# Performance work log

Measured on AMD Instinct MI355X. Metric: run time of the kernel, lower is better.

The kernel has to match this reference:

```python
import jax, jax.numpy as jnp
import numpy as np

EPS = 1e-8
N = 4
B = 1_000_000


def setup_inputs() -> dict:
    key = jax.random.key(0)
    g = jax.random.normal(key, (B, N, N), dtype=jnp.float32)
    # SPD covariance-like matrices: G G^T + 0.1 I (well-conditioned, distinct eigvals)
    x = jnp.einsum('bik,bjk->bij', g, g) / N + 0.1 * jnp.eye(N, dtype=jnp.float32)
    return {"x": x}


def reference(x):
    # 1) symmetrize + epsilon regularization (ensure SPD)
    sym = 0.5 * (x + jnp.swapaxes(x, -1, -2)) + EPS * jnp.eye(N, dtype=x.dtype)
    # 2) exact matrix log via eigendecomposition
    w, v = jnp.linalg.eigh(sym)                      # w: [B, N], v: [B, N, N]
    log_w = jnp.log(jnp.maximum(w, EPS))
    logm = jnp.einsum('bik,bk,bjk->bij', v, log_w, v)  # V diag(log w) V^T
    # 3) re-symmetrize
    logm = 0.5 * (logm + jnp.swapaxes(logm, -1, -2))
    # 4) upper-triangular vectorization, row-major (i, j>=i) order
    iu, ju = jnp.triu_indices(N)
    return logm[:, iu, ju]                           # [B, N*(N+1)//2]
```

## Files before the change

### kernel.cpp

```cpp
#include <hip/hip_runtime.h>
#include <math.h>

#ifndef NSWEEP
#define NSWEEP 4
#endif

#define EPSV 1e-8f

__device__ __forceinline__ float fast_sqrtf(float x) {
#if __has_builtin(__builtin_amdgcn_sqrtf)
  return __builtin_amdgcn_sqrtf(x);
#else
  return sqrtf(x);
#endif
}
__device__ __forceinline__ float fast_rcpf(float x) {
#if __has_builtin(__builtin_amdgcn_rcpf)
  return __builtin_amdgcn_rcpf(x);
#else
  return 1.0f / x;
#endif
}
__device__ __forceinline__ float fast_rsqf(float x) {
#if __has_builtin(__builtin_amdgcn_rsqf)
  return __builtin_amdgcn_rsqf(x);
#else
  return rsqrtf(x);
#endif
}
__device__ __forceinline__ float fast_logf(float x) {
#if __has_builtin(__builtin_amdgcn_logf)
  return __builtin_amdgcn_logf(x) * 0.6931471805599453f;
#else
  return logf(x);
#endif
}

#define JROT(APP, AQQ, APQ, AK1P, AK1Q, AK2P, AK2Q,                       \
             VP0, VQ0, VP1, VQ1, VP2, VQ2, VP3, VQ3)                      \
  do {                                                                    \
    float a_ = APQ;                                                       \
    float d_ = AQQ - APP;                                                 \
    float a2_ = a_ + a_;                                                  \
    float r_ = fast_sqrtf(fmaf(d_, d_, a2_ * a2_));                       \
    float den_ = fmaxf(fabsf(d_) + r_, 1e-30f);                          \
    float num_ = __int_as_float(__float_as_int(a2_) ^                     \
                                (__float_as_int(d_) & 0x80000000));       \
    float t_ = num_ * fast_rcpf(den_);                                    \
    float c_ = fast_rsqf(fmaf(t_, t_, 1.0f));                             \
    float s_ = t_ * c_;                                                   \
    float ta_ = t_ * a_;                                                  \
    APP = APP - ta_;                                                      \
    AQQ = AQQ + ta_;                                                      \
    APQ = 0.0f;                                                           \
    { float kp_ = AK1P, kq_ = AK1Q;                                       \
      AK1P = fmaf(c_, kp_, -s_ * kq_);                                    \
      AK1Q = fmaf(s_, kp_, c_ * kq_); }                                   \
    { float kp_ = AK2P, kq_ = AK2Q;                                       \
      AK2P = fmaf(c_, kp_, -s_ * kq_);                                    \
      AK2Q = fmaf(s_, kp_, c_ * kq_); }                                   \
    { float p_ = VP0, q_ = VQ0;                                           \
      VP0 = fmaf(c_, p_, -s_ * q_);                                       \
      VQ0 = fmaf(s_, p_, c_ * q_); }                                      \
    { float p_ = VP1, q_ = VQ1;                                           \
      VP1 = fmaf(c_, p_, -s_ * q_);                                       \
      VQ1 = fmaf(s_, p_, c_ * q_); }                                      \
    { float p_ = VP2, q_ = VQ2;                                           \
      VP2 = fmaf(c_, p_, -s_ * q_);                                       \
      VQ2 = fmaf(s_, p_, c_ * q_); }                                      \
    { float p_ = VP3, q_ = VQ3;                                           \
      VP3 = fmaf(c_, p_, -s_ * q_);                                       \
      VQ3 = fmaf(s_, p_, c_ * q_); }                                      \
  } while (0)

__device__ __forceinline__ void logm_one(float4 r0, float4 r1, float4 r2,
                                         float4 r3, float o[10]) {
  float a00 = r0.x + EPSV;
  float a01 = 0.5f * (r0.y + r1.x);
  float a02 = 0.5f * (r0.z + r2.x);
  float a03 = 0.5f * (r0.w + r3.x);
  float a11 = r1.y + EPSV;
  float a12 = 0.5f * (r1.z + r2.y);
  float a13 = 0.5f * (r1.w + r3.y);
  float a22 = r2.z + EPSV;
  float a23 = 0.5f * (r2.w + r3.z);
  float a33 = r3.w + EPSV;

  float v00 = 1.f, v01 = 0.f, v02 = 0.f, v03 = 0.f;
  float v10 = 0.f, v11 = 1.f, v12 = 0.f, v13 = 0.f;
  float v20 = 0.f, v21 = 0.f, v22 = 1.f, v23 = 0.f;
  float v30 = 0.f, v31 = 0.f, v32 = 0.f, v33 = 1.f;

#pragma unroll 1
  for (int sweep = 0; sweep < NSWEEP; ++sweep) {
    JROT(a00, a11, a01, a02, a12, a03, a13,
         v00, v01, v10, v11, v20, v21, v30, v31);
    JROT(a00, a22, a02, a01, a12, a03, a23,
         v00, v02, v10, v12, v20, v22, v30, v32);
    JROT(a00, a33, a03, a01, a13, a02, a23,
         v00, v03, v10, v13, v20, v23, v30, v33);
    JROT(a11, a22, a12, a01, a02, a13, a23,
         v01, v02, v11, v12, v21, v22, v31, v32);
    JROT(a11, a33, a13, a01, a03, a12, a23,
         v01, v03, v11, v13, v21, v23, v31, v33);
    JROT(a22, a33, a23, a02, a03, a12, a13,
         v02, v03, v12, v13, v22, v23, v32, v33);
  }

  float lw0 = fast_logf(fmaxf(a00, EPSV));
  float lw1 = fast_logf(fmaxf(a11, EPSV));
  float lw2 = fast_logf(fmaxf(a22, EPSV));
  float lw3 = fast_logf(fmaxf(a33, EPSV));

  float w00 = v00 * lw0, w01 = v01 * lw1, w02 = v02 * lw2, w03 = v03 * lw3;
  float w10 = v10 * lw0, w11 = v11 * lw1, w12 = v12 * lw2, w13 = v13 * lw3;
  float w20 = v20 * lw0, w21 = v21 * lw1, w22 = v22 * lw2, w23 = v23 * lw3;
  float w30 = v30 * lw0, w31 = v31 * lw1, w32 = v32 * lw2, w33 = v33 * lw3;

  o[0] = fmaf(w00, v00, fmaf(w01, v01, fmaf(w02, v02, w03 * v03)));
  o[1] = fmaf(w00, v10, fmaf(w01, v11, fmaf(w02, v12, w03 * v13)));
  o[2] = fmaf(w00, v20, fmaf(w01, v21, fmaf(w02, v22, w03 * v23)));
  o[3] = fmaf(w00, v30, fmaf(w01, v31, fmaf(w02, v32, w03 * v33)));
  o[4] = fmaf(w10, v10, fmaf(w11, v11, fmaf(w12, v12, w13 * v13)));
  o[5] = fmaf(w10, v20, fmaf(w11, v21, fmaf(w12, v22, w13 * v23)));
  o[6] = fmaf(w10, v30, fmaf(w11, v31, fmaf(w12, v32, w13 * v33)));
  o[7] = fmaf(w20, v20, fmaf(w21, v21, fmaf(w22, v22, w23 * v23)));
  o[8] = fmaf(w20, v30, fmaf(w21, v31, fmaf(w22, v32, w23 * v33)));
  o[9] = fmaf(w30, v30, fmaf(w31, v31, fmaf(w32, v32, w33 * v33)));
}

__global__ __launch_bounds__(256) void TangentSpaceLayer_64141041598486_kernel(
    const float* __restrict__ x, float* __restrict__ out, int B) {
  __shared__ __align__(16) float so[512 * 10];
  const int t = threadIdx.x;
  const int base = blockIdx.x * 512;
  const int m0 = min(base + t, B - 1);
  const int m1 = min(base + 256 + t, B - 1);

  const float* p0 = x + (size_t)m0 * 16;
  const float* p1 = x + (size_t)m1 * 16;
  float4 a0 = *(const float4*)(p0 + 0);
  float4 a1 = *(const float4*)(p0 + 4);
  float4 a2 = *(const float4*)(p0 + 8);
  float4 a3 = *(const float4*)(p0 + 12);
  float4 b0 = *(const float4*)(p1 + 0);
  float4 b1 = *(const float4*)(p1 + 4);
  float4 b2 = *(const float4*)(p1 + 8);
  float4 b3 = *(const float4*)(p1 + 12);

  float oA[10], oB[10];
  logm_one(a0, a1, a2, a3, oA);
  logm_one(b0, b1, b2, b3, oB);

  float* spA = so + t * 10;
  float* spB = so + (t + 256) * 10;
#pragma unroll
  for (int i = 0; i < 10; ++i) spA[i] = oA[i];
#pragma unroll
  for (int i = 0; i < 10; ++i) spB[i] = oB[i];

  __syncthreads();

  const int valid = min(512, B - blockIdx.x * 512);
  const int nf = valid * 10;
  const int n4 = nf >> 2;
  float* obase = out + (size_t)blockIdx.x * 5120;
  const float4* s4 = (const float4*)so;
  float4* o4 = (float4*)obase;
  for (int i = t; i < n4; i += 256) o4[i] = s4[i];
  for (int i = n4 * 4 + t; i < nf; i += 256) obase[i] = so[i];
}

extern "C" void kernel_launch(void* const* d_in, const int* in_sizes, int n_in,
                              void* d_out, int out_size, void* d_ws, size_t ws_size,
                              hipStream_t stream) {
  const float* x = (const float*)d_in[0];
  float* out = (float*)d_out;
  const int B = in_sizes[0] / 16;
  const int blocks = (B + 511) / 512;
  hipLaunchKernelGGL(TangentSpaceLayer_64141041598486_kernel, dim3(blocks),
                     dim3(256), 0, stream, x, out, B);
}
```

Measured before the change: 113.4 us.

## Interleave three matrices per thread and use rsqrt-only Jacobi rotation

Each thread now processes three 4x4 matrices instead of two, and each Jacobi rotation step is interleaved across the three matrices to expose independent instruction-level parallelism. The rotation formula is also rewritten to derive c and s from two reciprocal square roots, replacing the sqrt and rcp calls. This aims to hide transcendental latency and cut the cost per rotation. In exchange it raises register pressure (about 78 live floats per thread), launches fewer blocks, and uses a larger shared-memory staging buffer.

```diff
diff --git a/kernel.cpp b/kernel.cpp
--- a/kernel.cpp
+++ b/kernel.cpp
@@ -6,21 +6,10 @@
 #endif
 
 #define EPSV 1e-8f
+#define NM 3
+#define BT 256
+#define MPB (NM * BT)
 
-__device__ __forceinline__ float fast_sqrtf(float x) {
-#if __has_builtin(__builtin_amdgcn_sqrtf)
-  return __builtin_amdgcn_sqrtf(x);
-#else
-  return sqrtf(x);
-#endif
-}
-__device__ __forceinline__ float fast_rcpf(float x) {
-#if __has_builtin(__builtin_amdgcn_rcpf)
-  return __builtin_amdgcn_rcpf(x);
-#else
-  return 1.0f / x;
-#endif
-}
 __device__ __forceinline__ float fast_rsqf(float x) {
 #if __has_builtin(__builtin_amdgcn_rsqf)
   return __builtin_amdgcn_rsqf(x);
@@ -36,139 +25,149 @@
 #endif
 }
 
-#define JROT(APP, AQQ, APQ, AK1P, AK1Q, AK2P, AK2Q,                       \
-             VP0, VQ0, VP1, VQ1, VP2, VQ2, VP3, VQ3)                      \
-  do {                                                                    \
-    float a_ = APQ;                                                       \
-    float d_ = AQQ - APP;                                                 \
-    float a2_ = a_ + a_;                                                  \
-    float r_ = fast_sqrtf(fmaf(d_, d_, a2_ * a2_));                       \
-    float den_ = fmaxf(fabsf(d_) + r_, 1e-30f);                          \
-    float num_ = __int_as_float(__float_as_int(a2_) ^                     \
-                                (__float_as_int(d_) & 0x80000000));       \
-    float t_ = num_ * fast_rcpf(den_);                                    \
-    float c_ = fast_rsqf(fmaf(t_, t_, 1.0f));                             \
-    float s_ = t_ * c_;                                                   \
-    float ta_ = t_ * a_;                                                  \
-    APP = APP - ta_;                                                      \
-    AQQ = AQQ + ta_;                                                      \
-    APQ = 0.0f;                                                           \
-    { float kp_ = AK1P, kq_ = AK1Q;                                       \
-      AK1P = fmaf(c_, kp_, -s_ * kq_);                                    \
-      AK1Q = fmaf(s_, kp_, c_ * kq_); }                                   \
-    { float kp_ = AK2P, kq_ = AK2Q;                                       \
-      AK2P = fmaf(c_, kp_, -s_ * kq_);                                    \
-      AK2Q = fmaf(s_, kp_, c_ * kq_); }                                   \
-    { float p_ = VP0, q_ = VQ0;                                           \
-      VP0 = fmaf(c_, p_, -s_ * q_);                                       \
-      VQ0 = fmaf(s_, p_, c_ * q_); }                                      \
-    { float p_ = VP1, q_ = VQ1;                                           \
-      VP1 = fmaf(c_, p_, -s_ * q_);                                       \
-      VQ1 = fmaf(s_, p_, c_ * q_); }                                      \
-    { float p_ = VP2, q_ = VQ2;                                           \
-      VP2 = fmaf(c_, p_, -s_ * q_);                                       \
-      VQ2 = fmaf(s_, p_, c_ * q_); }                                      \
-    { float p_ = VP3, q_ = VQ3;                                           \
-      VP3 = fmaf(c_, p_, -s_ * q_);                                       \
-      VQ3 = fmaf(s_, p_, c_ * q_); }                                      \
+#define JROT(APP, AQQ, APQ, AK1P, AK1Q, AK2P, AK2Q,                         \
+             VP0, VQ0, VP1, VQ1, VP2, VQ2, VP3, VQ3)                        \
+  do {                                                                      \
+    float aa_ = APQ;                                                        \
+    float d_ = AQQ - APP;                                                   \
+    float a2_ = aa_ + aa_;                                                  \
+    float r2_ = fmaf(d_, d_, a2_ * a2_);                                    \
+    float h_ = fast_rsqf(fmaxf(r2_, 1e-30f));                               \
+    float p_ = fabsf(d_) * h_;                                              \
+    p_ = (r2_ <= 1e-30f) ? 1.0f : p_;                                       \
+    float q_ = fmaf(2.0f, p_, 2.0f);                                        \
+    float ri_ = fast_rsqf(q_);                                              \
+    float c_ = q_ * (0.5f * ri_);                                           \
+    float n_ = __int_as_float(__float_as_int(a2_ * h_) ^                    \
+                              (__float_as_int(d_) & 0x80000000));           \
+    float s_ = n_ * ri_;                                                    \
+    float t_ = (n_ + n_) * (ri_ * ri_);                                     \
+    float ta_ = t_ * aa_;                                                   \
+    APP = APP - ta_;                                                        \
+    AQQ = AQQ + ta_;                                                        \
+    APQ = 0.0f;                                                             \
+    { float kp_ = AK1P, kq_ = AK1Q;                                         \
+      AK1P = fmaf(c_, kp_, -s_ * kq_);                                      \
+      AK1Q = fmaf(s_, kp_, c_ * kq_); }                                     \
+    { float kp_ = AK2P, kq_ = AK2Q;                                         \
+      AK2P = fmaf(c_, kp_, -s_ * kq_);                                      \
+      AK2Q = fmaf(s_, kp_, c_ * kq_); }                                     \
+    { float p0_ = VP0, q0_ = VQ0;                                           \
+      VP0 = fmaf(c_, p0_, -s_ * q0_);                                       \
+      VQ0 = fmaf(s_, p0_, c_ * q0_); }                                      \
+    { float p0_ = VP1, q0_ = VQ1;                                           \
+      VP1 = fmaf(c_, p0_, -s_ * q0_);                                       \
+      VQ1 = fmaf(s_, p0_, c_ * q0_); }                                      \
+    { float p0_ = VP2, q0_ = VQ2;                                           \
+      VP2 = fmaf(c_, p0_, -s_ * q0_);                                       \
+      VQ2 = fmaf(s_, p0_, c_ * q0_); }                                      \
+    { float p0_ = VP3, q0_ = VQ3;                                           \
+      VP3 = fmaf(c_, p0_, -s_ * q0_);                                       \
+      VQ3 = fmaf(s_, p0_, c_ * q0_); }                                      \
   } while (0)
 
-__device__ __forceinline__ void logm_one(float4 r0, float4 r1, float4 r2,
-                                         float4 r3, float o[10]) {
-  float a00 = r0.x + EPSV;
-  float a01 = 0.5f * (r0.y + r1.x);
-  float a02 = 0.5f * (r0.z + r2.x);
-  float a03 = 0.5f * (r0.w + r3.x);
-  float a11 = r1.y + EPSV;
-  float a12 = 0.5f * (r1.z + r2.y);
-  float a13 = 0.5f * (r1.w + r3.y);
-  float a22 = r2.z + EPSV;
-  float a23 = 0.5f * (r2.w + r3.z);
-  float a33 = r3.w + EPSV;
+#define ROT_01(m) JROT(A[m][0], A[m][4], A[m][1], A[m][2], A[m][5],         \
+                       A[m][3], A[m][6], V[m][0], V[m][1], V[m][4],         \
+                       V[m][5], V[m][8], V[m][9], V[m][12], V[m][13])
+#define ROT_02(m) JROT(A[m][0], A[m][7], A[m][2], A[m][1], A[m][5],         \
+                       A[m][3], A[m][8], V[m][0], V[m][2], V[m][4],         \
+                       V[m][6], V[m][8], V[m][10], V[m][12], V[m][14])
+#define ROT_03(m) JROT(A[m][0], A[m][9], A[m][3], A[m][1], A[m][6],         \
+                       A[m][2], A[m][8], V[m][0], V[m][3], V[m][4],         \
+                       V[m][7], V[m][8], V[m][11], V[m][12], V[m][15])
+#define ROT_12(m) JROT(A[m][4], A[m][7], A[m][5], A[m][1], A[m][2],         \
+                       A[m][6], A[m][8], V[m][1], V[m][2], V[m][5],         \
+                       V[m][6], V[m][9], V[m][10], V[m][13], V[m][14])
+#define ROT_13(m) JROT(A[m][4], A[m][9], A[m][6], A[m][1], A[m][3],         \
+                       A[m][5], A[m][8], V[m][1], V[m][3], V[m][5],         \
+                       V[m][7], V[m][9], V[m][11], V[m][13], V[m][15])
+#define ROT_23(m) JROT(A[m][7], A[m][9], A[m][8], A[m][2], A[m][3],         \
+                       A[m][5], A[m][6], V[m][2], V[m][3], V[m][6],         \
+                       V[m][7], V[m][10], V[m][11], V[m][14], V[m][15])
 
-  float v00 = 1.f, v01 = 0.f, v02 = 0.f, v03 = 0.f;
-  float v10 = 0.f, v11 = 1.f, v12 = 0.f, v13 = 0.f;
-  float v20 = 0.f, v21 = 0.f, v22 = 1.f, v23 = 0.f;
-  float v30 = 0.f, v31 = 0.f, v32 = 0.f, v33 = 1.f;
+__global__ __launch_bounds__(256) void TangentSpaceLayer_64141041598486_kernel(
+    const float* __restrict__ x, float* __restrict__ out, int B) {
+  __shared__ __align__(16) float so[MPB * 10];
+  const int t = threadIdx.x;
+  const int base = blockIdx.x * MPB;
+
+  float A[NM][10];
+  float V[NM][16];
+
+#pragma unroll
+  for (int m = 0; m < NM; ++m) {
+    const int idx = min(base + m * BT + t, B - 1);
+    const float4* p = (const float4*)(x + (size_t)idx * 16);
+    float4 r0 = p[0], r1 = p[1], r2 = p[2], r3 = p[3];
+    A[m][0] = r0.x + EPSV;
+    A[m][1] = 0.5f * (r0.y + r1.x);
+    A[m][2] = 0.5f * (r0.z + r2.x);
+    A[m][3] = 0.5f * (r0.w + r3.x);
+    A[m][4] = r1.y + EPSV;
+    A[m][5] = 0.5f * (r1.z + r2.y);
+    A[m][6] = 0.5f * (r1.w + r3.y);
+    A[m][7] = r2.z + EPSV;
+    A[m][8] = 0.5f * (r2.w + r3.z);
+    A[m][9] = r3.w + EPSV;
+#pragma unroll
+    for (int i = 0; i < 16; ++i) V[m][i] = (i % 5 == 0) ? 1.0f : 0.0f;
+  }
 
 #pragma unroll 1
   for (int sweep = 0; sweep < NSWEEP; ++sweep) {
-    JROT(a00, a11, a01, a02, a12, a03, a13,
-         v00, v01, v10, v11, v20, v21, v30, v31);
-    JROT(a00, a22, a02, a01, a12, a03, a23,
-         v00, v02, v10, v12, v20, v22, v30, v32);
-    JROT(a00, a33, a03, a01, a13, a02, a23,
-         v00, v03, v10, v13, v20, v23, v30, v33);
-    JROT(a11, a22, a12, a01, a02, a13, a23,
-         v01, v02, v11, v12, v21, v22, v31, v32);
-    JROT(a11, a33, a13, a01, a03, a12, a23,
-         v01, v03, v11, v13, v21, v23, v31, v33);
-    JROT(a22, a33, a23, a02, a03, a12, a13,
-         v02, v03, v12, v13, v22, v23, v32, v33);
+#pragma unroll
+    for (int m = 0; m < NM; ++m) ROT_01(m);
+#pragma unroll
+    for (int m = 0; m < NM; ++m) ROT_02(m);
+#pragma unroll
+    for (int m = 0; m < NM; ++m) ROT_03(m);
+#pragma unroll
+    for (int m = 0; m < NM; ++m) ROT_12(m);
+#pragma unroll
+    for (int m = 0; m < NM; ++m) ROT_13(m);
+#pragma unroll
+    for (int m = 0; m < NM; ++m) ROT_23(m);
   }
 
-  float lw0 = fast_logf(fmaxf(a00, EPSV));
-  float lw1 = fast_logf(fmaxf(a11, EPSV));
-  float lw2 = fast_logf(fmaxf(a22, EPSV));
-  float lw3 = fast_logf(fmaxf(a33, EPSV));
+#pragma unroll
+  for (int m = 0; m < NM; ++m) {
+    float lw0 = fast_logf(fmaxf(A[m][0], EPSV));
+    float lw1 = fast_logf(fmaxf(A[m][4], EPSV));
+    float lw2 = fast_logf(fmaxf(A[m][7], EPSV));
+    float lw3 = fast_logf(fmaxf(A[m][9], EPSV));
 
-  float w00 = v00 * lw0, w01 = v01 * lw1, w02 = v02 * lw2, w03 = v03 * lw3;
-  float w10 = v10 * lw0, w11 = v11 * lw1, w12 = v12 * lw2, w13 = v13 * lw3;
-  float w20 = v20 * lw0, w21 = v21 * lw1, w22 = v22 * lw2, w23 = v23 * lw3;
-  float w30 = v30 * lw0, w31 = v31 * lw1, w32 = v32 * lw2, w33 = v33 * lw3;
+    float w00 = V[m][0] * lw0, w01 = V[m][1] * lw1, w02 = V[m][2] * lw2,
+          w03 = V[m][3] * lw3;
+    float w10 = V[m][4] * lw0, w11 = V[m][5] * lw1, w12 = V[m][6] * lw2,
+          w13 = V[m][7] * lw3;
+    float w20 = V[m][8] * lw0, w21 = V[m][9] * lw1, w22 = V[m][10] * lw2,
+          w23 = V[m][11] * lw3;
+    float w30 = V[m][12] * lw0, w31 = V[m][13] * lw1, w32 = V[m][14] * lw2,
+          w33 = V[m][15] * lw3;
 
-  o[0] = fmaf(w00, v00, fmaf(w01, v01, fmaf(w02, v02, w03 * v03)));
-  o[1] = fmaf(w00, v10, fmaf(w01, v11, fmaf(w02, v12, w03 * v13)));
-  o[2] = fmaf(w00, v20, fmaf(w01, v21, fmaf(w02, v22, w03 * v23)));
-  o[3] = fmaf(w00, v30, fmaf(w01, v31, fmaf(w02, v32, w03 * v33)));
-  o[4] = fmaf(w10, v10, fmaf(w11, v11, fmaf(w12, v12, w13 * v13)));
-  o[5] = fmaf(w10, v20, fmaf(w11, v21, fmaf(w12, v22, w13 * v23)));
-  o[6] = fmaf(w10, v30, fmaf(w11, v31, fmaf(w12, v32, w13 * v33)));
-  o[7] = fmaf(w20, v20, fmaf(w21, v21, fmaf(w22, v22, w23 * v23)));
-  o[8] = fmaf(w20, v30, fmaf(w21, v31, fmaf(w22, v32, w23 * v33)));
-  o[9] = fmaf(w30, v30, fmaf(w31, v31, fmaf(w32, v32, w33 * v33)));
-}
-
-__global__ __launch_bounds__(256) void TangentSpaceLayer_64141041598486_kernel(
-    const float* __restrict__ x, float* __restrict__ out, int B) {
-  __shared__ __align__(16) float so[512 * 10];
-  const int t = threadIdx.x;
-  const int base = blockIdx.x * 512;
-  const int m0 = min(base + t, B - 1);
-  const int m1 = min(base + 256 + t, B - 1);
-
-  const float* p0 = x + (size_t)m0 * 16;
-  const float* p1 = x + (size_t)m1 * 16;
-  float4 a0 = *(const float4*)(p0 + 0);
-  float4 a1 = *(const float4*)(p0 + 4);
-  float4 a2 = *(const float4*)(p0 + 8);
-  float4 a3 = *(const float4*)(p0 + 12);
-  float4 b0 = *(const float4*)(p1 + 0);
-  float4 b1 = *(const float4*)(p1 + 4);
-  float4 b2 = *(const float4*)(p1 + 8);
-  float4 b3 = *(const float4*)(p1 + 12);
-
-  float oA[10], oB[10];
-  logm_one(a0, a1, a2, a3, oA);
-  logm_one(b0, b1, b2, b3, oB);
-
-  float* spA = so + t * 10;
-  float* spB = so + (t + 256) * 10;
-#pragma unroll
-  for (int i = 0; i < 10; ++i) spA[i] = oA[i];
-#pragma unroll
-  for (int i = 0; i < 10; ++i) spB[i] = oB[i];
+    float* sp = so + (m * BT + t) * 10;
+    sp[0] = fmaf(w00, V[m][0], fmaf(w01, V[m][1], fmaf(w02, V[m][2], w03 * V[m][3])));
+    sp[1] = fmaf(w00, V[m][4], fmaf(w01, V[m][5], fmaf(w02, V[m][6], w03 * V[m][7])));
+    sp[2] = fmaf(w00, V[m][8], fmaf(w01, V[m][9], fmaf(w02, V[m][10], w03 * V[m][11])));
+    sp[3] = fmaf(w00, V[m][12], fmaf(w01, V[m][13], fmaf(w02, V[m][14], w03 * V[m][15])));
+    sp[4] = fmaf(w10, V[m][4], fmaf(w11, V[m][5], fmaf(w12, V[m][6], w13 * V[m][7])));
+    sp[5] = fmaf(w10, V[m][8], fmaf(w11, V[m][9], fmaf(w12, V[m][10], w13 * V[m][11])));
+    sp[6] = fmaf(w10, V[m][12], fmaf(w11, V[m][13], fmaf(w12, V[m][14], w13 * V[m][15])));
+    sp[7] = fmaf(w20, V[m][8], fmaf(w21, V[m][9], fmaf(w22, V[m][10], w23 * V[m][11])));
+    sp[8] = fmaf(w20, V[m][12], fmaf(w21, V[m][13], fmaf(w22, V[m][14], w23 * V[m][15])));
+    sp[9] = fmaf(w30, V[m][12], fmaf(w31, V[m][13], fmaf(w32, V[m][14], w33 * V[m][15])));
+  }
 
   __syncthreads();
 
-  const int valid = min(512, B - blockIdx.x * 512);
+  const int valid = min(MPB, B - base);
   const int nf = valid * 10;
   const int n4 = nf >> 2;
-  float* obase = out + (size_t)blockIdx.x * 5120;
+  float* obase = out + (size_t)base * 10;
   const float4* s4 = (const float4*)so;
   float4* o4 = (float4*)obase;
-  for (int i = t; i < n4; i += 256) o4[i] = s4[i];
-  for (int i = n4 * 4 + t; i < nf; i += 256) obase[i] = so[i];
+  for (int i = t; i < n4; i += BT) o4[i] = s4[i];
+  for (int i = n4 * 4 + t; i < nf; i += BT) obase[i] = so[i];
 }
 
 extern "C" void kernel_launch(void* const* d_in, const int* in_sizes, int n_in,
@@ -177,7 +176,7 @@
   const float* x = (const float*)d_in[0];
   float* out = (float*)d_out;
   const int B = in_sizes[0] / 16;
-  const int blocks = (B + 511) / 512;
+  const int blocks = (B + MPB - 1) / MPB;
   hipLaunchKernelGGL(TangentSpaceLayer_64141041598486_kernel, dim3(blocks),
-                     dim3(256), 0, stream, x, out, B);
+                     dim3(BT), 0, stream, x, out, B);
 }
```

Result: slower. 117.4 us (+3.5%).
